# Optimization experiments

Hardware: AMD Instinct MI355X
Metric: run time of the kernel (lower is better)

The kernel has to match this reference:

```python
import jax, jax.numpy as jnp
import numpy as np

N, E, IN_DIM, H, C = 100000, 1600000, 128, 4, 64
NEG_SLOPE = 0.2
BN_EPS = 1e-5


def setup_inputs() -> dict:
    key = jax.random.key(0)
    ks = jax.random.split(key, 9)
    s = 1.0 / np.sqrt(IN_DIM)
    return {
        "feature": jax.random.normal(ks[0], (N, IN_DIM), dtype=jnp.float32),
        "edge_index": jax.random.randint(ks[1], (2, E), 0, N, dtype=jnp.int64),
        "W_l": jax.random.uniform(ks[2], (IN_DIM, H * C), jnp.float32, -s, s),
        "b_l": jnp.zeros((H * C,), jnp.float32),
        "W_r": jax.random.uniform(ks[3], (IN_DIM, H * C), jnp.float32, -s, s),
        "b_r": jnp.zeros((H * C,), jnp.float32),
        "att": jax.random.normal(ks[4], (H, C), dtype=jnp.float32) * 0.1,
        "bias": jnp.zeros((H * C,), jnp.float32),
        "gamma": jnp.ones((H * C,), jnp.float32),
        "beta": jnp.zeros((H * C,), jnp.float32),
    }


def reference(feature, edge_index, W_l, b_l, W_r, b_r, att, bias, gamma, beta):
    n = feature.shape[0]
    # add self loops (add_self_loops=True)
    loops = jnp.arange(n, dtype=edge_index.dtype)
    src = jnp.concatenate([edge_index[0], loops])
    dst = jnp.concatenate([edge_index[1], loops])
    # GATv2: separate source/target linear projections -> [N, H, C]
    x_l = (feature @ W_l + b_l).reshape(n, H, C)
    x_r = (feature @ W_r + b_r).reshape(n, H, C)
    # per-edge attention score: a^T LeakyReLU(x_l[src] + x_r[dst])  [Etot, H]
    e = jax.nn.leaky_relu(x_l[src] + x_r[dst], NEG_SLOPE)
    alpha = jnp.einsum('ehc,hc->eh', e, att)
    # segment softmax over incoming edges per target node
    amax = jax.ops.segment_max(alpha, dst, num_segments=n)  # [N, H]
    alpha = jnp.exp(alpha - amax[dst])
    denom = jax.ops.segment_sum(alpha, dst, num_segments=n)  # [N, H]
    alpha = alpha / (denom[dst] + 1e-16)
    # weighted scatter-aggregate of source messages
    out = jax.ops.segment_sum(x_l[src] * alpha[:, :, None], dst, num_segments=n)
    out = out.reshape(n, H * C) + bias  # concat=True
    # BatchNorm1d (training: batch statistics over nodes)
    mean = out.mean(axis=0)
    var = out.var(axis=0)
    out = (out - mean) / jnp.sqrt(var + BN_EPS) * gamma + beta
    return jax.nn.relu(out)
```

## Files before the change

kernel.cpp:

```cpp
#include <hip/hip_runtime.h>
#include <cstdint>

#define IN_DIM 128
#define HC 256
#define NEG_SLOPE 0.2f
#define BN_EPS 1e-5f
#define LOG2E 1.44269504088896340736f

#define B_HIST 1536
#define B_FILL 1024
#define NBUF 64

typedef short bf16x8 __attribute__((ext_vector_type(8)));
typedef float f32x4 __attribute__((ext_vector_type(4)));

#define EXP2F(x) __builtin_amdgcn_exp2f(x)

__device__ __forceinline__ unsigned short f2bf(float f) {
    union { float f; unsigned int u; } v; v.f = f;
    unsigned int r = (v.u + 0x7FFFu + ((v.u >> 16) & 1u)) >> 16;
    return (unsigned short)r;
}
__device__ __forceinline__ float bf2f(unsigned short h) {
    union { unsigned int u; float f; } v; v.u = ((unsigned int)h) << 16;
    return v.f;
}

template<int CTRL>
__device__ __forceinline__ float dppadd(float x) {
    int y = __builtin_amdgcn_update_dpp(0, __builtin_bit_cast(int, x), CTRL, 0xF, 0xF, true);
    return x + __builtin_bit_cast(float, y);
}
__device__ __forceinline__ float red16(float p) {
    p = dppadd<0xB1>(p);
    p = dppadd<0x4E>(p);
    p = dppadd<0x124>(p);
    p = dppadd<0x128>(p);
    return p;
}

__device__ __forceinline__ void unpk(ushort4 u, float* f) {
    f[0] = bf2f(u.x); f[1] = bf2f(u.y); f[2] = bf2f(u.z); f[3] = bf2f(u.w);
}
__device__ __forceinline__ float esc(const float* f, float x0, float x1, float x2, float x3,
                                     float4 a) {
    float z0 = f[0] + x0, z1 = f[1] + x1, z2 = f[2] + x2, z3 = f[3] + x3;
    float p = a.x * fmaxf(z0, NEG_SLOPE * z0);
    p = fmaf(a.y, fmaxf(z1, NEG_SLOPE * z1), p);
    p = fmaf(a.z, fmaxf(z2, NEG_SLOPE * z2), p);
    p = fmaf(a.w, fmaxf(z3, NEG_SLOPE * z3), p);
    return p;
}

__global__ __launch_bounds__(256) void prep(
    const float* __restrict__ Wl, const float* __restrict__ Wr,
    unsigned short* __restrict__ Wfrag,
    int* __restrict__ cnt, float* __restrict__ partials, int n)
{
    int b = blockIdx.x;
    if (b < 32) {
        int ob = b * 4 + (threadIdx.x >> 6);
        int j = ob >> 2;
        int kk = ob & 3;
        int l = threadIdx.x & 63;
        int col = j * 16 + (l & 15);
        const float* W = (col < 256) ? Wl : Wr;
        int c = col & 255;
        unsigned short tmp[8];
#pragma unroll
        for (int m = 0; m < 8; ++m) {
            int k = kk * 32 + ((l >> 4) << 3) + m;
            tmp[m] = f2bf(W[(size_t)k * 256 + c]);
        }
        ulonglong2* dst = (ulonglong2*)(Wfrag + ((size_t)(j * 4 + kk) * 64 + l) * 8);
        *dst = *(ulonglong2*)tmp;
    } else {
        int idx = (b - 32) * 256 + threadIdx.x;
        int stride = 96 * 256;
        for (int i = idx; i < n; i += stride) cnt[i] = 0;
        for (int i = idx; i < NBUF * 1024; i += stride) partials[i] = 0.f;
    }
}

__global__ __launch_bounds__(256) void phase_hg(
    const float* __restrict__ F, const unsigned short* __restrict__ Wfrag,
    const float* __restrict__ bl, const float* __restrict__ br,
    unsigned short* __restrict__ xl, unsigned short* __restrict__ xr,
    const int* __restrict__ ei, int* __restrict__ cnt, int* __restrict__ rank,
    int E, int n, int ntiles)
{
    int b = blockIdx.x;
    if (b < B_HIST) {
        for (int e = b * 256 + threadIdx.x; e < E; e += B_HIST * 256) {
            int dst = ei[(size_t)E + e];
            rank[e] = atomicAdd(&cnt[dst], 1);
        }
        return;
    }
    int i = (b - B_HIST) * 4 + (threadIdx.x >> 6);
    if (i >= ntiles) return;
    int l = threadIdx.x & 63;

    int row = i * 16 + (l & 15);
    bf16x8 afr[4];
#pragma unroll
    for (int kk = 0; kk < 4; ++kk) {
        int k0 = kk * 32 + ((l >> 4) << 3);
        float4 f0 = make_float4(0.f, 0.f, 0.f, 0.f), f1 = f0;
        if (row < n) {
            const float* p = F + (size_t)row * IN_DIM + k0;
            f0 = *(const float4*)p;
            f1 = *(const float4*)(p + 4);
        }
        unsigned short tmp[8];
        tmp[0] = f2bf(f0.x); tmp[1] = f2bf(f0.y); tmp[2] = f2bf(f0.z); tmp[3] = f2bf(f0.w);
        tmp[4] = f2bf(f1.x); tmp[5] = f2bf(f1.y); tmp[6] = f2bf(f1.z); tmp[7] = f2bf(f1.w);
        afr[kk] = *(bf16x8*)tmp;
    }

    const bf16x8* wv = (const bf16x8*)Wfrag + l;
    int cl = l & 15;
    int rbase = i * 16 + ((l >> 4) << 2);

#pragma unroll 4
    for (int j = 0; j < 32; ++j) {
        const bf16x8* bp = wv + (size_t)j * 4 * 64;
        f32x4 acc = {0.f, 0.f, 0.f, 0.f};
        acc = __builtin_amdgcn_mfma_f32_16x16x32_bf16(afr[0], bp[0 * 64], acc, 0, 0, 0);
        acc = __builtin_amdgcn_mfma_f32_16x16x32_bf16(afr[1], bp[1 * 64], acc, 0, 0, 0);
        acc = __builtin_amdgcn_mfma_f32_16x16x32_bf16(afr[2], bp[2 * 64], acc, 0, 0, 0);
        acc = __builtin_amdgcn_mfma_f32_16x16x32_bf16(afr[3], bp[3 * 64], acc, 0, 0, 0);

        int col = j * 16 + cl;
        unsigned short* X = (col < 256) ? xl : xr;
        int c = col & 255;
        float bv = (col < 256) ? bl[c] : br[c];
#pragma unroll
        for (int q = 0; q < 4; ++q) {
            int r = rbase + q;
            if (r < n) X[(size_t)r * HC + c] = f2bf(acc[q] + bv);
        }
    }
}

#define SCAN_BLOCKS 256

__global__ __launch_bounds__(256) void scan_phaseA(const int* __restrict__ cnt,
                                                   int* __restrict__ blocksums,
                                                   int n, int ept)
{
    __shared__ int red[256];
    int t = threadIdx.x;
    int g = blockIdx.x * 256 + t;
    int beg = g * ept, end = min(beg + ept, n);
    int s = 0;
    for (int i = beg; i < end; ++i) s += cnt[i];
    red[t] = s;
    __syncthreads();
    for (int d = 128; d > 0; d >>= 1) {
        if (t < d) red[t] += red[t + d];
        __syncthreads();
    }
    if (t == 0) blocksums[blockIdx.x] = red[0];
}

__global__ __launch_bounds__(256) void scan_phaseC(const int* __restrict__ cnt,
                                                   const int* __restrict__ blocksums,
                                                   int* __restrict__ off,
                                                   int n, int ept)
{
    __shared__ int bs[256];
    __shared__ int sums[256];
    int t = threadIdx.x;
    bs[t] = blocksums[t];
    int g = blockIdx.x * 256 + t;
    int beg = g * ept, end = min(beg + ept, n);
    int s = 0;
    for (int i = beg; i < end; ++i) s += cnt[i];
    sums[t] = s;
    __syncthreads();
    for (int d = 1; d < 256; d <<= 1) {
        int v1 = (t >= d) ? sums[t - d] : 0;
        int v2 = (t >= d) ? bs[t - d] : 0;
        __syncthreads();
        sums[t] += v1;
        bs[t] += v2;
        __syncthreads();
    }
    int blockoff = (blockIdx.x == 0) ? 0 : bs[blockIdx.x - 1];
    int run = blockoff + ((t == 0) ? 0 : sums[t - 1]);
    for (int i = beg; i < end; ++i) {
        int c = cnt[i];
        off[i] = run;
        run += c;
    }
    if (blockIdx.x == 0 && t == 0) off[n] = bs[255];
}

__global__ void fill_kernel(const int* __restrict__ ei, const int* __restrict__ rank,
                            const int* __restrict__ off, int* __restrict__ csr_boff,
                            int E)
{
    for (int e = blockIdx.x * blockDim.x + threadIdx.x; e < E;
         e += gridDim.x * blockDim.x) {
        int src = ei[e];
        int dst = ei[(size_t)E + e];
        int pos = off[dst] + rank[e];
        csr_boff[pos] = src << 9;
    }
}

__global__ __launch_bounds__(256) void gat_agg(
    const unsigned short* __restrict__ xl, const unsigned short* __restrict__ xr,
    const int* __restrict__ csr_boff, const int* __restrict__ off,
    const float* __restrict__ att, const float* __restrict__ bias,
    unsigned short* __restrict__ outb, float* __restrict__ partials, int n)
{
    int w = threadIdx.x >> 6;
    int d = blockIdx.x * 4 + w;
    int lane = threadIdx.x & 63;
    bool active = (d < n);

    float vx = 0.f, vy = 0.f, vz = 0.f, vw = 0.f;

    if (active) {
        const char* xlc = (const char*)xl;
        int lo8 = lane << 3;
        ushort4 xru = ((const ushort4*)xr)[(size_t)d * 64 + lane];
        float xr0 = bf2f(xru.x), xr1 = bf2f(xru.y), xr2 = bf2f(xru.z), xr3 = bf2f(xru.w);
        float4 att4 = *(const float4*)(att + 4 * lane);
        att4.x *= LOG2E; att4.y *= LOG2E; att4.z *= LOG2E; att4.w *= LOG2E;

        int beg = __builtin_amdgcn_readfirstlane(off[d]);
        int end = __builtin_amdgcn_readfirstlane(off[d + 1]);

        float ax, ay, az, aw, lsum;
        {
            ushort4 t0 = *(const ushort4*)(xlc + ((size_t)d << 9) + lo8);
            float f0[4];
            unpk(t0, f0);
            float p0 = esc(f0, xr0, xr1, xr2, xr3, att4);
            p0 = red16(p0);
            float e0 = EXP2F(p0);
            ax = e0 * f0[0]; ay = e0 * f0[1]; az = e0 * f0[2]; aw = e0 * f0[3];
            lsum = e0;
        }

        int nmain = (end - beg) & ~3;
        int imend = beg + nmain;
        int i = beg;

        ushort4 u0, u1, u2, u3;
        if (i < imend) {
            int b0 = __builtin_amdgcn_readfirstlane(csr_boff[i]);
            int b1 = __builtin_amdgcn_readfirstlane(csr_boff[i + 1]);
            int b2 = __builtin_amdgcn_readfirstlane(csr_boff[i + 2]);
            int b3 = __builtin_amdgcn_readfirstlane(csr_boff[i + 3]);
            u0 = *(const ushort4*)(xlc + b0 + lo8);
            u1 = *(const ushort4*)(xlc + b1 + lo8);
            u2 = *(const ushort4*)(xlc + b2 + lo8);
            u3 = *(const ushort4*)(xlc + b3 + lo8);
        }
        while (i < imend) {
            ushort4 c0 = u0, c1 = u1, c2 = u2, c3 = u3;
            int inext = i + 4;
            if (inext < imend) {
                int b0 = __builtin_amdgcn_readfirstlane(csr_boff[inext]);
                int b1 = __builtin_amdgcn_readfirstlane(csr_boff[inext + 1]);
                int b2 = __builtin_amdgcn_readfirstlane(csr_boff[inext + 2]);
                int b3 = __builtin_amdgcn_readfirstlane(csr_boff[inext + 3]);
                u0 = *(const ushort4*)(xlc + b0 + lo8);
                u1 = *(const ushort4*)(xlc + b1 + lo8);
                u2 = *(const ushort4*)(xlc + b2 + lo8);
                u3 = *(const ushort4*)(xlc + b3 + lo8);
            }
            float f0[4], f1[4], f2[4], f3[4];
            unpk(c0, f0); unpk(c1, f1); unpk(c2, f2); unpk(c3, f3);

            float p0 = esc(f0, xr0, xr1, xr2, xr3, att4);
            float p1 = esc(f1, xr0, xr1, xr2, xr3, att4);
            float p2 = esc(f2, xr0, xr1, xr2, xr3, att4);
            float p3 = esc(f3, xr0, xr1, xr2, xr3, att4);

            p0 = dppadd<0xB1>(p0);  p1 = dppadd<0xB1>(p1);  p2 = dppadd<0xB1>(p2);  p3 = dppadd<0xB1>(p3);
            p0 = dppadd<0x4E>(p0);  p1 = dppadd<0x4E>(p1);  p2 = dppadd<0x4E>(p2);  p3 = dppadd<0x4E>(p3);
            p0 = dppadd<0x124>(p0); p1 = dppadd<0x124>(p1); p2 = dppadd<0x124>(p2); p3 = dppadd<0x124>(p3);
            p0 = dppadd<0x128>(p0); p1 = dppadd<0x128>(p1); p2 = dppadd<0x128>(p2); p3 = dppadd<0x128>(p3);

            float e0 = EXP2F(p0), e1 = EXP2F(p1);
            float e2 = EXP2F(p2), e3 = EXP2F(p3);
            ax = fmaf(e0, f0[0], fmaf(e1, f1[0], fmaf(e2, f2[0], fmaf(e3, f3[0], ax))));
            ay = fmaf(e0, f0[1], fmaf(e1, f1[1], fmaf(e2, f2[1], fmaf(e3, f3[1], ay))));
            az = fmaf(e0, f0[2], fmaf(e1, f1[2], fmaf(e2, f2[2], fmaf(e3, f3[2], az))));
            aw = fmaf(e0, f0[3], fmaf(e1, f1[3], fmaf(e2, f2[3], fmaf(e3, f3[3], aw))));
            lsum += (e0 + e1) + (e2 + e3);
            i = inext;
        }
        for (; i < end; ++i) {
            int b0 = __builtin_amdgcn_readfirstlane(csr_boff[i]);
            ushort4 t0 = *(const ushort4*)(xlc + b0 + lo8);
            float f0[4];
            unpk(t0, f0);
            float p0 = esc(f0, xr0, xr1, xr2, xr3, att4);
            p0 = red16(p0);
            float e0 = EXP2F(p0);
            ax = fmaf(e0, f0[0], ax); ay = fmaf(e0, f0[1], ay);
            az = fmaf(e0, f0[2], az); aw = fmaf(e0, f0[3], aw);
            lsum += e0;
        }

        float inv = 1.f / (lsum + 1e-16f);
        float4 b4 = *(const float4*)(bias + 4 * lane);
        vx = fmaf(ax, inv, b4.x);
        vy = fmaf(ay, inv, b4.y);
        vz = fmaf(az, inv, b4.z);
        vw = fmaf(aw, inv, b4.w);
        ushort4 o;
        o.x = f2bf(vx); o.y = f2bf(vy); o.z = f2bf(vz); o.w = f2bf(vw);
        ((ushort4*)outb)[(size_t)d * 64 + lane] = o;
        vx = bf2f(o.x); vy = bf2f(o.y); vz = bf2f(o.z); vw = bf2f(o.w);
    }

    __shared__ float sv[4 * 512];
    int c0 = (lane << 2);
    float* svw = sv + w * 512;
    svw[c0 + 0] = vx; svw[c0 + 1] = vy; svw[c0 + 2] = vz; svw[c0 + 3] = vw;
    svw[256 + c0 + 0] = vx * vx; svw[256 + c0 + 1] = vy * vy;
    svw[256 + c0 + 2] = vz * vz; svw[256 + c0 + 3] = vw * vw;
    __syncthreads();
    int t = threadIdx.x;
    float S = sv[t] + sv[512 + t] + sv[1024 + t] + sv[1536 + t];
    float Q = sv[256 + t] + sv[768 + t] + sv[1280 + t] + sv[1792 + t];
    float* pb = partials + (size_t)(blockIdx.x & (NBUF - 1)) * 1024;
    atomicAdd(&pb[t], S);
    atomicAdd(&pb[512 + t], Q);
}

__global__ __launch_bounds__(256) void bn_final(const float* __restrict__ partials,
                                                float* __restrict__ stats, int n)
{
    int c = threadIdx.x;
    float s = 0.f, s2 = 0.f;
    for (int b = 0; b < NBUF; ++b) {
        s  += partials[(size_t)b * 1024 + c];
        s2 += partials[(size_t)b * 1024 + 512 + c];
    }
    float mean = s / (float)n;
    float var = s2 / (float)n - mean * mean;
    stats[c] = mean;
    stats[256 + c] = rsqrtf(var + BN_EPS);
}

__global__ void bn_apply(const unsigned short* __restrict__ outb,
                         const float* __restrict__ stats,
                         const float* __restrict__ gamma, const float* __restrict__ beta,
                         float* __restrict__ out, long long total4)
{
    long long stride = (long long)gridDim.x * blockDim.x;
    for (long long i = blockIdx.x * (long long)blockDim.x + threadIdx.x; i < total4;
         i += stride) {
        int cb = ((int)(i & 63)) * 4;
        ushort4 u = ((const ushort4*)outb)[i];
        float4 o;
        o.x = fmaxf(0.f, (bf2f(u.x) - stats[cb + 0]) * stats[256 + cb + 0] * gamma[cb + 0] + beta[cb + 0]);
        o.y = fmaxf(0.f, (bf2f(u.y) - stats[cb + 1]) * stats[256 + cb + 1] * gamma[cb + 1] + beta[cb + 1]);
        o.z = fmaxf(0.f, (bf2f(u.z) - stats[cb + 2]) * stats[256 + cb + 2] * gamma[cb + 2] + beta[cb + 2]);
        o.w = fmaxf(0.f, (bf2f(u.w) - stats[cb + 3]) * stats[256 + cb + 3] * gamma[cb + 3] + beta[cb + 3]);
        ((float4*)out)[i] = o;
    }
}

extern "C" void kernel_launch(void* const* d_in, const int* in_sizes, int n_in,
                              void* d_out, int out_size, void* d_ws, size_t ws_size,
                              hipStream_t stream)
{
    const float* feature = (const float*)d_in[0];
    const int* ei        = (const int*)d_in[1];
    const float* Wl   = (const float*)d_in[2];
    const float* bl   = (const float*)d_in[3];
    const float* Wr   = (const float*)d_in[4];
    const float* br   = (const float*)d_in[5];
    const float* att  = (const float*)d_in[6];
    const float* bias = (const float*)d_in[7];
    const float* gamma = (const float*)d_in[8];
    const float* beta  = (const float*)d_in[9];

    const int n = in_sizes[0] / IN_DIM;
    const int E = in_sizes[1] / 2;
    const int ntiles = (n + 15) / 16;

    char* ws = (char*)d_ws;
    size_t o = 0;
    auto carve = [&](size_t bytes) -> void* {
        void* p = ws + o; o = (o + bytes + 15) & ~(size_t)15; return p;
    };
    unsigned short* xl    = (unsigned short*)carve((size_t)n * HC * sizeof(short));
    unsigned short* xr    = (unsigned short*)carve((size_t)n * HC * sizeof(short));
    unsigned short* outb  = (unsigned short*)carve((size_t)n * HC * sizeof(short));
    unsigned short* Wfrag = (unsigned short*)carve((size_t)32 * 4 * 64 * 8 * sizeof(short));
    int*   csr_boff = (int*)carve((size_t)E * sizeof(int));
    int*   rank    = (int*)carve((size_t)E * sizeof(int));
    int*   cnt     = (int*)carve((size_t)n * sizeof(int));
    int*   off     = (int*)carve((size_t)(n + 1) * sizeof(int));
    int*   blocksums = (int*)carve(SCAN_BLOCKS * sizeof(int));
    float* partials = (float*)carve((size_t)NBUF * 1024 * sizeof(float));
    float* stats   = (float*)carve(512 * sizeof(float));
    float* outf = (float*)d_out;

    if (o > ws_size) return;

    prep<<<128, 256, 0, stream>>>(Wl, Wr, Wfrag, cnt, partials, n);

    phase_hg<<<B_HIST + (ntiles + 3) / 4, 256, 0, stream>>>(
        feature, Wfrag, bl, br, xl, xr, ei, cnt, rank, E, n, ntiles);

    int ept = (n + SCAN_BLOCKS * 256 - 1) / (SCAN_BLOCKS * 256);
    scan_phaseA<<<SCAN_BLOCKS, 256, 0, stream>>>(cnt, blocksums, n, ept);
    scan_phaseC<<<SCAN_BLOCKS, 256, 0, stream>>>(cnt, blocksums, off, n, ept);

    fill_kernel<<<B_FILL, 256, 0, stream>>>(ei, rank, off, csr_boff, E);

    int agg_blocks = (n + 3) / 4;
    gat_agg<<<agg_blocks, 256, 0, stream>>>(xl, xr, csr_boff, off, att, bias,
                                            outb, partials, n);

    bn_final<<<1, 256, 0, stream>>>(partials, stats, n);
    long long total4 = (long long)n * (HC / 4);
    bn_apply<<<4096, 256, 0, stream>>>(outb, stats, gamma, beta, outf, total4);
}
```

Measured before the change: 345.5 us.

## Make GAT aggregation a persistent grid-stride kernel with per-wave BN accumulation

The aggregation kernel now launches a fixed grid of 2048 blocks, and each wave loops over destination nodes with a grid stride instead of handling exactly one node. The loop-invariant att and bias loads are hoisted out of that loop. BatchNorm sums and sums of squares are kept in registers per wave and flushed with atomics once at the end, which removes the per-block shared-memory reduction and the per-block atomics. Atomic traffic drops from about 25k blocks to 8k waves, though each wave issues 8 atomics per lane. Static striding may load-balance worse on skewed degree distributions.

```diff
diff --git a/kernel.cpp b/kernel.cpp
--- a/kernel.cpp
+++ b/kernel.cpp
@@ -10,6 +10,7 @@
 #define B_HIST 1536
 #define B_FILL 1024
 #define NBUF 64
+#define B_AGG 2048
 
 typedef short bf16x8 __attribute__((ext_vector_type(8)));
 typedef float f32x4 __attribute__((ext_vector_type(4)));
@@ -216,20 +217,22 @@
     const float* __restrict__ att, const float* __restrict__ bias,
     unsigned short* __restrict__ outb, float* __restrict__ partials, int n)
 {
-    int w = threadIdx.x >> 6;
-    int d = blockIdx.x * 4 + w;
+    int gwave = blockIdx.x * 4 + (threadIdx.x >> 6);
+    int nwaves = B_AGG * 4;
     int lane = threadIdx.x & 63;
-    bool active = (d < n);
-
-    float vx = 0.f, vy = 0.f, vz = 0.f, vw = 0.f;
-
-    if (active) {
-        const char* xlc = (const char*)xl;
-        int lo8 = lane << 3;
+
+    const char* xlc = (const char*)xl;
+    int lo8 = lane << 3;
+    float4 att4 = *(const float4*)(att + 4 * lane);
+    att4.x *= LOG2E; att4.y *= LOG2E; att4.z *= LOG2E; att4.w *= LOG2E;
+    float4 b4 = *(const float4*)(bias + 4 * lane);
+
+    float bnS0 = 0.f, bnS1 = 0.f, bnS2 = 0.f, bnS3 = 0.f;
+    float bnQ0 = 0.f, bnQ1 = 0.f, bnQ2 = 0.f, bnQ3 = 0.f;
+
+    for (int d = gwave; d < n; d += nwaves) {
         ushort4 xru = ((const ushort4*)xr)[(size_t)d * 64 + lane];
         float xr0 = bf2f(xru.x), xr1 = bf2f(xru.y), xr2 = bf2f(xru.z), xr3 = bf2f(xru.w);
-        float4 att4 = *(const float4*)(att + 4 * lane);
-        att4.x *= LOG2E; att4.y *= LOG2E; att4.z *= LOG2E; att4.w *= LOG2E;
 
         int beg = __builtin_amdgcn_readfirstlane(off[d]);
         int end = __builtin_amdgcn_readfirstlane(off[d + 1]);
@@ -310,30 +313,28 @@
         }
 
         float inv = 1.f / (lsum + 1e-16f);
-        float4 b4 = *(const float4*)(bias + 4 * lane);
-        vx = fmaf(ax, inv, b4.x);
-        vy = fmaf(ay, inv, b4.y);
-        vz = fmaf(az, inv, b4.z);
-        vw = fmaf(aw, inv, b4.w);
         ushort4 o;
-        o.x = f2bf(vx); o.y = f2bf(vy); o.z = f2bf(vz); o.w = f2bf(vw);
+        o.x = f2bf(fmaf(ax, inv, b4.x));
+        o.y = f2bf(fmaf(ay, inv, b4.y));
+        o.z = f2bf(fmaf(az, inv, b4.z));
+        o.w = f2bf(fmaf(aw, inv, b4.w));
         ((ushort4*)outb)[(size_t)d * 64 + lane] = o;
-        vx = bf2f(o.x); vy = bf2f(o.y); vz = bf2f(o.z); vw = bf2f(o.w);
-    }
-
-    __shared__ float sv[4 * 512];
-    int c0 = (lane << 2);
-    float* svw = sv + w * 512;
-    svw[c0 + 0] = vx; svw[c0 + 1] = vy; svw[c0 + 2] = vz; svw[c0 + 3] = vw;
-    svw[256 + c0 + 0] = vx * vx; svw[256 + c0 + 1] = vy * vy;
-    svw[256 + c0 + 2] = vz * vz; svw[256 + c0 + 3] = vw * vw;
-    __syncthreads();
-    int t = threadIdx.x;
-    float S = sv[t] + sv[512 + t] + sv[1024 + t] + sv[1536 + t];
-    float Q = sv[256 + t] + sv[768 + t] + sv[1280 + t] + sv[1792 + t];
-    float* pb = partials + (size_t)(blockIdx.x & (NBUF - 1)) * 1024;
-    atomicAdd(&pb[t], S);
-    atomicAdd(&pb[512 + t], Q);
+        float vx = bf2f(o.x), vy = bf2f(o.y), vz = bf2f(o.z), vw = bf2f(o.w);
+        bnS0 += vx; bnS1 += vy; bnS2 += vz; bnS3 += vw;
+        bnQ0 = fmaf(vx, vx, bnQ0); bnQ1 = fmaf(vy, vy, bnQ1);
+        bnQ2 = fmaf(vz, vz, bnQ2); bnQ3 = fmaf(vw, vw, bnQ3);
+    }
+
+    float* pb = partials + (size_t)(gwave & (NBUF - 1)) * 1024;
+    int c0 = lane << 2;
+    atomicAdd(&pb[c0 + 0], bnS0);
+    atomicAdd(&pb[c0 + 1], bnS1);
+    atomicAdd(&pb[c0 + 2], bnS2);
+    atomicAdd(&pb[c0 + 3], bnS3);
+    atomicAdd(&pb[512 + c0 + 0], bnQ0);
+    atomicAdd(&pb[512 + c0 + 1], bnQ1);
+    atomicAdd(&pb[512 + c0 + 2], bnQ2);
+    atomicAdd(&pb[512 + c0 + 3], bnQ3);
 }
 
 __global__ __launch_bounds__(256) void bn_final(const float* __restrict__ partials,
@@ -420,9 +421,8 @@
 
     fill_kernel<<<B_FILL, 256, 0, stream>>>(ei, rank, off, csr_boff, E);
 
-    int agg_blocks = (n + 3) / 4;
-    gat_agg<<<agg_blocks, 256, 0, stream>>>(xl, xr, csr_boff, off, att, bias,
-                                            outb, partials, n);
+    gat_agg<<<B_AGG, 256, 0, stream>>>(xl, xr, csr_boff, off, att, bias,
+                                       outb, partials, n);
 
     bn_final<<<1, 256, 0, stream>>>(partials, stats, n);
     long long total4 = (long long)n * (HC / 4);
```

Measured after the change: 387.5 us. 1.12x slower.
